# Kernel optimization log

Hardware: AMD Instinct MI355X
Metric: run time of the kernel (lower is better)

Reference implementation:

```python
import jax, jax.numpy as jnp
import numpy as np

B, C, N, K, G = 8, 64, 2048, 20, 64  # batch, in-channels, points, knn k, growth
BN_EPS = 1e-5


def setup_inputs() -> dict:
    key = jax.random.key(0)
    ks = jax.random.split(key, 8)
    def w(k_, fan_in, out):
        return jax.random.normal(k_, (out, fan_in), dtype=jnp.float32) / np.sqrt(fan_in)
    return {
        "inputs": jax.random.normal(ks[0], (B, C, N, 1), dtype=jnp.float32),
        "W1": w(ks[1], 2 * C, G), "b1": jnp.zeros((G,), jnp.float32),
        "g1": jnp.ones((G,), jnp.float32), "be1": jnp.zeros((G,), jnp.float32),
        "W2": w(ks[2], 2 * (C + G), G), "b2": jnp.zeros((G,), jnp.float32),
        "g2": jnp.ones((G,), jnp.float32), "be2": jnp.zeros((G,), jnp.float32),
        "W3": w(ks[3], 2 * (C + 2 * G), G), "b3": jnp.zeros((G,), jnp.float32),
        "g3": jnp.ones((G,), jnp.float32), "be3": jnp.zeros((G,), jnp.float32),
    }


def _knn_idx(x, k):
    # x: (B, C, N). Negative squared pairwise distance, topk = k nearest (incl. self).
    sq = jnp.sum(x * x, axis=1)                       # (B, N)
    inner = jnp.einsum('bcn,bcm->bnm', x, x)          # (B, N, N)
    neg_dist = 2.0 * inner - sq[:, :, None] - sq[:, None, :]
    return jax.lax.top_k(neg_dist, k)[1]              # (B, N, k)


def _dyn_edge_block(x4, W, b, gamma, beta):
    # x4: (B, Cin, N, 1) -> (B, G, N, 1). Dynamic KNN + EdgeConv + BN(batch stats) + ReLU + max over k.
    x = x4[..., 0]                                    # (B, Cin, N)
    idx = _knn_idx(x, K)                              # (B, N, K)
    xj = jax.vmap(lambda xb, ib: xb[:, ib])(x, idx)   # (B, Cin, N, K)
    xi = x[..., None]                                 # (B, Cin, N, 1)
    e = jnp.concatenate([jnp.broadcast_to(xi, xj.shape), xj - xi], axis=1)  # (B, 2Cin, N, K)
    y = jnp.einsum('oc,bcnk->bonk', W, e) + b[None, :, None, None]
    mu = jnp.mean(y, axis=(0, 2, 3), keepdims=True)
    var = jnp.var(y, axis=(0, 2, 3), keepdims=True)
    y = gamma[None, :, None, None] * (y - mu) * jax.lax.rsqrt(var + BN_EPS) + beta[None, :, None, None]
    y = jax.nn.relu(y)
    return jnp.max(y, axis=3, keepdims=True)          # (B, G, N, 1)


def reference(inputs, W1, b1, g1, be1, W2, b2, g2, be2, W3, b3, g3, be3):
    f = _dyn_edge_block(inputs, W1, b1, g1, be1)      # (B, G, N, 1)
    f1 = jnp.concatenate([f, inputs], axis=1)         # (B, C+G, N, 1)
    f2_new = _dyn_edge_block(f1, W2, b2, g2, be2)
    f2 = jnp.concatenate([f2_new, f1], axis=1)        # (B, C+2G, N, 1)
    f3_new = _dyn_edge_block(f2, W3, b3, g3, be3)
    return jnp.concatenate([f3_new, f2], axis=1)      # (B, C+3G, N, 1)
```

## Files before the change

### kernel.cpp

```cpp
#include <hip/hip_runtime.h>

#define NB 8
#define NPTS 2048
#define KNN 20
#define OUTC 256
#define NPB 8
#define NRED 64

__global__ void k_copy_in(const float* __restrict__ in, float* __restrict__ out) {
    int t = blockIdx.x * 256 + threadIdx.x;
    int n = t & (NPTS - 1);
    int c = (t >> 11) & 63;
    int b = t >> 17;
    out[((size_t)b * OUTC + 192 + c) * NPTS + n] = in[t];
}

__global__ void k_prep_uv(const float* __restrict__ W, int Cin,
                          float* __restrict__ Ut, float* __restrict__ Vt) {
    int t = blockIdx.x * 256 + threadIdx.x;
    if (t >= Cin * 64) return;
    int o = t & 63;
    int c = t >> 6;
    float wa = W[o * (2 * Cin) + c];
    float wb = W[o * (2 * Cin) + Cin + c];
    Ut[c * 64 + o] = wa - wb;
    Vt[c * 64 + o] = wb;
}

__global__ void k_sqsum(const float* __restrict__ out, int Cin, float* __restrict__ sq) {
    int t = blockIdx.x * 256 + threadIdx.x;
    int b = t >> 11;
    int m = t & (NPTS - 1);
    const float* X = out + ((size_t)b * OUTC + (OUTC - Cin)) * NPTS;
    float s = 0.f;
    for (int c = 0; c < Cin; ++c) {
        float x = X[(size_t)c * NPTS + m];
        s = fmaf(x, x, s);
    }
    sq[t] = s;
}

#define BSW(j) (((j) >> 3) * 12 + ((j) & 7))

__global__ __launch_bounds__(256) void k_dist(const float* __restrict__ out, int Cin,
        const float* __restrict__ sq, float* __restrict__ dist,
        int bOff, int n0, int NR, int sym) {
    int mt, nt;
    if (sym) {
        int u = blockIdx.x;
        mt = 0;
        int rem = 16;
        while (u >= rem) { u -= rem; --rem; ++mt; }
        nt = mt + u;
    } else {
        mt = blockIdx.x; nt = blockIdx.y;
    }
    int bz = blockIdx.z;
    int b = bOff + bz;
    const float* X = out + ((size_t)b * OUTC + (OUTC - Cin)) * NPTS;
    int m0 = mt * 128;
    int nbase = n0 + nt * 128;
    __shared__ float An[16][128];
    __shared__ float Bm[16][192];
    int t = threadIdx.x;
    int tx = t & 15, ty = t >> 4;
    float acc[8][8];
    #pragma unroll
    for (int i = 0; i < 8; ++i)
        #pragma unroll
        for (int j = 0; j < 8; ++j) acc[i][j] = 0.f;

    int lcol = (t & 31) * 4;
    int swl = BSW(lcol);
    int lrow = t >> 5;
    for (int kk = 0; kk < Cin; kk += 16) {
        #pragma unroll
        for (int i = 0; i < 2; ++i) {
            int rr = lrow + i * 8;
            const float* src = X + (size_t)(kk + rr) * NPTS;
            *(float4*)&An[rr][lcol] = *(const float4*)&src[nbase + lcol];
            *(float4*)&Bm[rr][swl]  = *(const float4*)&src[m0 + lcol];
        }
        __syncthreads();
        #pragma unroll
        for (int k = 0; k < 16; ++k) {
            float av[8], bv[8];
            *(float4*)&av[0] = *(float4*)&An[k][ty * 8];
            *(float4*)&av[4] = *(float4*)&An[k][ty * 8 + 4];
            *(float4*)&bv[0] = *(float4*)&Bm[k][tx * 12];
            *(float4*)&bv[4] = *(float4*)&Bm[k][tx * 12 + 4];
            #pragma unroll
            for (int ia = 0; ia < 8; ++ia)
                #pragma unroll
                for (int ib = 0; ib < 8; ++ib)
                    acc[ia][ib] = fmaf(av[ia], bv[ib], acc[ia][ib]);
        }
        __syncthreads();
    }
    const float* sqb = sq + b * NPTS;
    float sqm[8];
    *(float4*)&sqm[0] = *(const float4*)&sqb[m0 + tx * 8];
    *(float4*)&sqm[4] = *(const float4*)&sqb[m0 + tx * 8 + 4];
    float* dbase = dist + (size_t)bz * NR * NPTS;
    #pragma unroll
    for (int ia = 0; ia < 8; ++ia) {
        int rn = nt * 128 + ty * 8 + ia;
        float ov[8];
        #pragma unroll
        for (int ib = 0; ib < 8; ++ib) ov[ib] = 2.f * acc[ia][ib] - sqm[ib];
        *(float4*)&dbase[(size_t)rn * NPTS + m0 + tx * 8]     = *(float4*)&ov[0];
        *(float4*)&dbase[(size_t)rn * NPTS + m0 + tx * 8 + 4] = *(float4*)&ov[4];
    }
    if (sym && mt < nt) {
        float sqn[8];
        *(float4*)&sqn[0] = *(const float4*)&sqb[nbase + ty * 8];
        *(float4*)&sqn[4] = *(const float4*)&sqb[nbase + ty * 8 + 4];
        #pragma unroll
        for (int ib = 0; ib < 8; ++ib) {
            int rm = m0 + tx * 8 + ib;
            float ov[8];
            #pragma unroll
            for (int ia = 0; ia < 8; ++ia) ov[ia] = 2.f * acc[ia][ib] - sqn[ia];
            *(float4*)&dbase[(size_t)rm * NPTS + nbase + ty * 8]     = *(float4*)&ov[0];
            *(float4*)&dbase[(size_t)rm * NPTS + nbase + ty * 8 + 4] = *(float4*)&ov[4];
        }
    }
}

#define SCOLX(lane, j) (((lane) << 2) + ((j) & 3) + (((j) >> 2) << 8))

__device__ __forceinline__ unsigned long long packkey(float v, int c) {
    unsigned u = __float_as_uint(v);
    u ^= ((unsigned)((int)u >> 31)) | 0x80000000u;
    return ((unsigned long long)u << 32) | (unsigned)(~c);
}

__device__ __forceinline__ void scan4k(const float (&v)[32], int lane,
        unsigned long long thrK,
        unsigned long long& a1, unsigned long long& a2,
        unsigned long long& a3, unsigned long long& a4, int& d) {
    unsigned long long tK = thrK;
    d = 0;
    #pragma unroll
    for (int p = 0; p < 4; ++p) {
        unsigned long long b0 = 0, b1 = 0, b2 = 0, b3 = 0;
        #pragma unroll
        for (int jj = 0; jj < 8; ++jj) {
            {
                int j = jj;
                unsigned long long kj = packkey(v[j], SCOLX(lane, j));
                if (kj < tK && kj > b0) b0 = kj;
            }
            {
                int j = 8 + jj;
                unsigned long long kj = packkey(v[j], SCOLX(lane, j));
                if (kj < tK && kj > b1) b1 = kj;
            }
            {
                int j = 16 + jj;
                unsigned long long kj = packkey(v[j], SCOLX(lane, j));
                if (kj < tK && kj > b2) b2 = kj;
            }
            {
                int j = 24 + jj;
                unsigned long long kj = packkey(v[j], SCOLX(lane, j));
                if (kj < tK && kj > b3) b3 = kj;
            }
        }
        if (b1 > b0) b0 = b1;
        if (b3 > b2) b2 = b3;
        if (b2 > b0) b0 = b2;
        if (p == 0)      a1 = b0;
        else if (p == 1) a2 = b0;
        else if (p == 2) a3 = b0;
        else             a4 = b0;
        if (b0 != 0) ++d;
        tK = b0;
    }
}

__global__ __launch_bounds__(256) void k_select(const float* __restrict__ dist,
        int* __restrict__ idx, int bOff, int n0, int NR) {
    int lane = threadIdx.x & 63;
    int r = blockIdx.x * 4 + (threadIdx.x >> 6);
    int bl = r / NR;
    int n = n0 + (r - bl * NR);
    const float4* row4 = (const float4*)(dist + (size_t)r * NPTS);
    float v[32];
    #pragma unroll
    for (int jj = 0; jj < 8; ++jj)
        *(float4*)&v[jj * 4] = row4[lane + 64 * jj];
    int* orow = idx + ((size_t)(bOff + bl) * NPTS + n) * KNN;

    unsigned long long a1, a2, a3, a4;
    int d;
    unsigned long long mlK = 0xFFFFFFFFFFFFFFFFull;
    scan4k(v, lane, mlK, a1, a2, a3, a4, d);

    for (int s = 0; s < KNN; ++s) {
        unsigned long long wk = a1;
        #pragma unroll
        for (int off = 32; off; off >>= 1) {
            unsigned long long ok = __shfl_xor(wk, off);
            if (ok > wk) wk = ok;
        }
        int wc = ~(int)(unsigned)(wk & 0xFFFFFFFFull);
        if (lane == 0) orow[s] = wc;
        bool won = (a1 != 0) && (wk == a1);
        if (won) {
            mlK = a1;
            a1 = a2; a2 = a3; a3 = a4; a4 = 0;
            --d;
        }
        if (s < KNN - 1 && __any(won && d == 0)) {
            if (won && d == 0)
                scan4k(v, lane, mlK, a1, a2, a3, a4, d);
        }
    }
}

__global__ __launch_bounds__(256) void k_pz(const float* __restrict__ out, int Cin,
        const float* __restrict__ Ut, const float* __restrict__ Vt,
        float* __restrict__ P, float* __restrict__ Z) {
    int b = blockIdx.y;
    int n0 = blockIdx.x * 64;
    const float* X = out + ((size_t)b * OUTC + (OUTC - Cin)) * NPTS;
    __shared__ float Xs[16][64];
    __shared__ float Us[16][64];
    __shared__ float Vs[16][64];
    int t = threadIdx.x;
    int tx = t & 15, ty = t >> 4;
    float accP[4][4] = {}, accZ[4][4] = {};
    int col = t & 63, r0 = t >> 6;
    for (int kk = 0; kk < Cin; kk += 16) {
        #pragma unroll
        for (int i = 0; i < 4; ++i) {
            int rr = r0 + i * 4;
            Xs[rr][col] = X[(size_t)(kk + rr) * NPTS + n0 + col];
            Us[rr][col] = Ut[(kk + rr) * 64 + col];
            Vs[rr][col] = Vt[(kk + rr) * 64 + col];
        }
        __syncthreads();
        #pragma unroll
        for (int k = 0; k < 16; ++k) {
            float xv[4], uv[4], vv[4];
            *(float4*)xv = *(float4*)&Xs[k][ty * 4];
            *(float4*)uv = *(float4*)&Us[k][tx * 4];
            *(float4*)vv = *(float4*)&Vs[k][tx * 4];
            #pragma unroll
            for (int a = 0; a < 4; ++a)
                #pragma unroll
                for (int o = 0; o < 4; ++o) {
                    accP[a][o] = fmaf(uv[o], xv[a], accP[a][o]);
                    accZ[a][o] = fmaf(vv[o], xv[a], accZ[a][o]);
                }
        }
        __syncthreads();
    }
    #pragma unroll
    for (int a = 0; a < 4; ++a) {
        size_t base = ((size_t)b * NPTS + n0 + ty * 4 + a) * 64 + tx * 4;
        *(float4*)&P[base] = *(float4*)&accP[a][0];
        *(float4*)&Z[base] = *(float4*)&accZ[a][0];
    }
}

__global__ __launch_bounds__(64) void k_gather(const int* __restrict__ idx,
        const float* __restrict__ P, const float* __restrict__ Z,
        const float* __restrict__ bias,
        float* __restrict__ ymax, float* __restrict__ ymin,
        float* __restrict__ partials) {
    int blk = blockIdx.x;
    int b = blk / (NPTS / NPB);
    int n0 = (blk % (NPTS / NPB)) * NPB;
    int o = threadIdx.x;
    float bv = bias[o];
    float S1 = 0.f, S2 = 0.f;
    const float* Zb = Z + (size_t)b * NPTS * 64;
    for (int i = 0; i < NPB; ++i) {
        int n = n0 + i;
        const int* ir = idx + ((size_t)b * NPTS + n) * KNN;
        float mx = -3.0e38f, mn = 3.0e38f, s1 = 0.f, s2 = 0.f;
        #pragma unroll
        for (int k = 0; k < KNN; ++k) {
            int m = ir[k];
            float zv = Zb[(size_t)m * 64 + o];
            mx = fmaxf(mx, zv);
            mn = fminf(mn, zv);
            s1 += zv;
            s2 = fmaf(zv, zv, s2);
        }
        float tv = P[((size_t)b * NPTS + n) * 64 + o] + bv;
        size_t yb = ((size_t)b * NPTS + n) * 64 + o;
        ymax[yb] = tv + mx;
        ymin[yb] = tv + mn;
        S1 += (float)KNN * tv + s1;
        S2 += fmaf((float)KNN * tv, tv, fmaf(2.f * tv, s1, s2));
    }
    partials[(size_t)blk * 128 + o] = S1;
    partials[(size_t)blk * 128 + 64 + o] = S2;
}

__global__ __launch_bounds__(256) void k_reduce(const float* __restrict__ partials,
                                                float* __restrict__ red) {
    __shared__ float L[256];
    int t = threadIdx.x;
    int j = t & 127, half = t >> 7;
    int rows = (NB * NPTS / NPB) / NRED;
    int base = blockIdx.x * rows + half;
    float s = 0.f;
    #pragma unroll
    for (int i = 0; i < 16; ++i)
        s += partials[(size_t)(base + 2 * i) * 128 + j];
    L[t] = s;
    __syncthreads();
    if (half == 0)
        red[(size_t)blockIdx.x * 128 + j] = L[j] + L[128 + j];
}

__global__ void k_stats(const float* __restrict__ red,
        const float* __restrict__ gamma, const float* __restrict__ beta,
        float* __restrict__ ss) {
    __shared__ float L[128];
    int j = threadIdx.x;
    float s = 0.f;
    #pragma unroll
    for (int p = 0; p < NRED; ++p) s += red[(size_t)p * 128 + j];
    L[j] = s;
    __syncthreads();
    if (j < 64) {
        const float cnt = (float)NB * NPTS * KNN;
        float mu = L[j] / cnt;
        float ms = L[64 + j] / cnt;
        float var = ms - mu * mu;
        float sc = gamma[j] / sqrtf(var + 1e-5f);
        ss[j] = sc;
        ss[64 + j] = beta[j] - mu * sc;
    }
}

__global__ __launch_bounds__(256) void k_final(const float* __restrict__ ymax,
        const float* __restrict__ ymin, const float* __restrict__ ss,
        float* __restrict__ out, int obase) {
    int b = blockIdx.y;
    int n0 = blockIdx.x * 64;
    __shared__ float T[64][65];
    int t = threadIdx.x;
    int o = t & 63, r0 = t >> 6;
    float sc = ss[o], sh = ss[64 + o];
    #pragma unroll
    for (int i = 0; i < 16; ++i) {
        int n = r0 + i * 4;
        size_t src = ((size_t)b * NPTS + n0 + n) * 64 + o;
        float v = (sc >= 0.f) ? ymax[src] : ymin[src];
        v = fmaf(sc, v, sh);
        T[o][n] = v > 0.f ? v : 0.f;
    }
    __syncthreads();
    #pragma unroll
    for (int i = 0; i < 16; ++i) {
        int oo = r0 + i * 4;
        out[((size_t)b * OUTC + obase + oo) * NPTS + n0 + o] = T[oo][o];
    }
}

extern "C" void kernel_launch(void* const* d_in, const int* in_sizes, int n_in,
                              void* d_out, int out_size, void* d_ws, size_t ws_size,
                              hipStream_t stream) {
    const float* inp   = (const float*)d_in[0];
    const float* W[3]  = {(const float*)d_in[1], (const float*)d_in[5], (const float*)d_in[9]};
    const float* bi[3] = {(const float*)d_in[2], (const float*)d_in[6], (const float*)d_in[10]};
    const float* ga[3] = {(const float*)d_in[3], (const float*)d_in[7], (const float*)d_in[11]};
    const float* be[3] = {(const float*)d_in[4], (const float*)d_in[8], (const float*)d_in[12]};
    float* out = (float*)d_out;
    (void)in_sizes; (void)n_in; (void)out_size;

    char* w = (char*)d_ws;
    size_t off = 0;
    auto alloc = [&](size_t bytes) -> void* {
        void* p = w + off;
        off = (off + bytes + 255) & ~(size_t)255;
        return p;
    };
    int*   idx      = (int*)  alloc((size_t)NB * NPTS * KNN * 4);
    float* Ut       = (float*)alloc(192 * 64 * 4);
    float* Vt       = (float*)alloc(192 * 64 * 4);
    float* sq       = (float*)alloc((size_t)NB * NPTS * 4);
    float* P        = (float*)alloc((size_t)NB * NPTS * 64 * 4);
    float* Z        = (float*)alloc((size_t)NB * NPTS * 64 * 4);
    float* ymax     = (float*)alloc((size_t)NB * NPTS * 64 * 4);
    float* ymin     = (float*)alloc((size_t)NB * NPTS * 64 * 4);
    float* partials = (float*)alloc((size_t)(NB * NPTS / NPB) * 128 * 4);
    float* red      = (float*)alloc((size_t)NRED * 128 * 4);
    float* ss       = (float*)alloc(128 * 4);

    float* dist = (float*)(w + off);
    size_t distAvail = (ws_size > off) ? (ws_size - off) : 0;
    const size_t matBytes = (size_t)NPTS * NPTS * 4;

    k_copy_in<<<NB * 64 * NPTS / 256, 256, 0, stream>>>(inp, out);

    int Cins[3]  = {64, 128, 192};
    int obase[3] = {128, 64, 0};
    int nblkGather = NB * NPTS / NPB;

    for (int l = 0; l < 3; ++l) {
        int Cin = Cins[l];
        k_prep_uv<<<(Cin * 64 + 255) / 256, 256, 0, stream>>>(W[l], Cin, Ut, Vt);
        k_sqsum<<<NB * NPTS / 256, 256, 0, stream>>>(out, Cin, sq);

        if (distAvail >= (size_t)NB * matBytes) {
            k_dist<<<dim3(136, 1, NB), 256, 0, stream>>>(out, Cin, sq, dist, 0, 0, NPTS, 1);
            k_select<<<NB * NPTS / 4, 256, 0, stream>>>(dist, idx, 0, 0, NPTS);
        } else if (distAvail >= matBytes) {
            for (int b = 0; b < NB; ++b) {
                k_dist<<<dim3(136, 1, 1), 256, 0, stream>>>(out, Cin, sq, dist, b, 0, NPTS, 1);
                k_select<<<NPTS / 4, 256, 0, stream>>>(dist, idx, b, 0, NPTS);
            }
        } else {
            int NR = (int)((distAvail / ((size_t)NPTS * 4)) & ~(size_t)127);
            if (NR < 128) NR = 128;
            for (int b = 0; b < NB; ++b) {
                for (int n0 = 0; n0 < NPTS; n0 += NR) {
                    int nr = (NPTS - n0 < NR) ? (NPTS - n0) : NR;
                    k_dist<<<dim3(16, nr / 128, 1), 256, 0, stream>>>(out, Cin, sq, dist, b, n0, nr, 0);
                    k_select<<<nr / 4, 256, 0, stream>>>(dist, idx, b, n0, nr);
                }
            }
        }

        k_pz<<<dim3(NPTS / 64, NB), 256, 0, stream>>>(out, Cin, Ut, Vt, P, Z);
        k_gather<<<nblkGather, 64, 0, stream>>>(idx, P, Z, bi[l], ymax, ymin, partials);
        k_reduce<<<NRED, 256, 0, stream>>>(partials, red);
        k_stats<<<1, 128, 0, stream>>>(red, ga[l], be[l], ss);
        k_final<<<dim3(NPTS / 64, NB), 256, 0, stream>>>(ymax, ymin, ss, out, obase[l]);
    }
}
```

Measured before the change: 616.1 us.

## Fuse distance GEMM with per-row top-k selection for first layer

For the first EdgeConv layer, a new kernel computes pairwise-distance tiles and keeps a running top-20 per row in shared memory, split across two column halves. A small merge kernel then combines the two partial top-20 lists into the final indices. This skips writing and re-reading the full N×N distance matrix. In exchange the insertion loop is serial and divergent, and the grid is small (512 blocks), so occupancy may be low.

```diff
diff --git a/kernel.cpp b/kernel.cpp
--- a/kernel.cpp
+++ b/kernel.cpp
@@ -216,6 +216,133 @@
             if (won && d == 0)
                 scan4k(v, lane, mlK, a1, a2, a3, a4, d);
         }
+    }
+}
+
+__global__ __launch_bounds__(256) void k_fdist(const float* __restrict__ out, int Cin,
+        const float* __restrict__ sq, unsigned long long* __restrict__ ptop) {
+    int rt = blockIdx.x;
+    int half = blockIdx.y;
+    int b = blockIdx.z;
+    const float* X = out + ((size_t)b * OUTC + (OUTC - Cin)) * NPTS;
+    int rbase = rt * 64;
+    __shared__ float An[16][64];
+    __shared__ float Bm[16][192];
+    __shared__ unsigned long long g20[64][20];
+    int t = threadIdx.x;
+    int tx = t & 15, ty = t >> 4;
+
+    for (int j = t; j < 64 * 20; j += 256) ((unsigned long long*)g20)[j] = 0ull;
+    __syncthreads();
+
+    const float* sqb = sq + b * NPTS;
+    int lcolA = (t & 15) * 4, lrowA = t >> 4;
+    int lcolB = (t & 31) * 4, lrowB = t >> 5;
+    int swlB = BSW(lcolB);
+
+    for (int mt = 0; mt < 8; ++mt) {
+        int m0 = half * 1024 + mt * 128;
+        float acc[4][8];
+        #pragma unroll
+        for (int i = 0; i < 4; ++i)
+            #pragma unroll
+            for (int j = 0; j < 8; ++j) acc[i][j] = 0.f;
+        for (int kk = 0; kk < Cin; kk += 16) {
+            __syncthreads();
+            *(float4*)&An[lrowA][lcolA] =
+                *(const float4*)&X[(size_t)(kk + lrowA) * NPTS + rbase + lcolA];
+            #pragma unroll
+            for (int i = 0; i < 2; ++i) {
+                int rr = lrowB + i * 8;
+                *(float4*)&Bm[rr][swlB] =
+                    *(const float4*)&X[(size_t)(kk + rr) * NPTS + m0 + lcolB];
+            }
+            __syncthreads();
+            #pragma unroll
+            for (int k = 0; k < 16; ++k) {
+                float av[4], bv[8];
+                *(float4*)&av[0] = *(float4*)&An[k][ty * 4];
+                *(float4*)&bv[0] = *(float4*)&Bm[k][tx * 12];
+                *(float4*)&bv[4] = *(float4*)&Bm[k][tx * 12 + 4];
+                #pragma unroll
+                for (int ia = 0; ia < 4; ++ia)
+                    #pragma unroll
+                    for (int ib = 0; ib < 8; ++ib)
+                        acc[ia][ib] = fmaf(av[ia], bv[ib], acc[ia][ib]);
+            }
+        }
+        float sqm[8];
+        *(float4*)&sqm[0] = *(const float4*)&sqb[m0 + tx * 8];
+        *(float4*)&sqm[4] = *(const float4*)&sqb[m0 + tx * 8 + 4];
+        int cb = m0 + tx * 8;
+        #pragma unroll
+        for (int ia = 0; ia < 4; ++ia) {
+            int row = ty * 4 + ia;
+            unsigned long long tl = ~0ull, h = 0ull;
+            #pragma unroll
+            for (int j = 0; j < 8; ++j) {
+                unsigned long long kj = packkey(2.f * acc[ia][j] - sqm[j], cb + j);
+                if (kj < tl && kj > h) h = kj;
+            }
+            while (true) {
+                unsigned long long w = h;
+                #pragma unroll
+                for (int off = 8; off; off >>= 1) {
+                    unsigned long long o = __shfl_xor(w, off);
+                    if (o > w) w = o;
+                }
+                unsigned long long c1 = g20[row][tx]; int s1 = tx;
+                if (tx < 4) {
+                    unsigned long long c2 = g20[row][16 + tx];
+                    if (c2 < c1) { c1 = c2; s1 = 16 + tx; }
+                }
+                #pragma unroll
+                for (int off = 8; off; off >>= 1) {
+                    unsigned long long oc = __shfl_xor(c1, off);
+                    int os = __shfl_xor(s1, off);
+                    if (oc < c1) { c1 = oc; s1 = os; }
+                }
+                if (w <= c1) break;
+                if (tx == 0) g20[row][s1] = w;
+                if (h == w && h != 0ull) {
+                    tl = h;
+                    h = 0ull;
+                    #pragma unroll
+                    for (int j = 0; j < 8; ++j) {
+                        unsigned long long kj = packkey(2.f * acc[ia][j] - sqm[j], cb + j);
+                        if (kj < tl && kj > h) h = kj;
+                    }
+                }
+            }
+        }
+    }
+    __syncthreads();
+    #pragma unroll
+    for (int ia = 0; ia < 4; ++ia) {
+        int row = ty * 4 + ia;
+        size_t base = ((size_t)b * NPTS + rbase + row) * 40 + (size_t)half * 20;
+        for (int j = tx; j < 20; j += 16)
+            ptop[base + j] = g20[row][j];
+    }
+}
+
+__global__ void k_kmerge(const unsigned long long* __restrict__ ptop,
+                         int* __restrict__ idx) {
+    int r = blockIdx.x * 256 + threadIdx.x;
+    const unsigned long long* src = ptop + (size_t)r * 40;
+    unsigned long long v[40];
+    #pragma unroll
+    for (int j = 0; j < 40; ++j) v[j] = src[j];
+    int* orow = idx + (size_t)r * KNN;
+    unsigned long long tV = ~0ull;
+    #pragma unroll 1
+    for (int s = 0; s < KNN; ++s) {
+        unsigned long long best = 0;
+        #pragma unroll
+        for (int j = 0; j < 40; ++j)
+            if (v[j] < tV && v[j] > best) best = v[j];
+        orow[s] = ~(int)(unsigned)(best & 0xFFFFFFFFull);
+        tV = best;
     }
 }
 
@@ -393,6 +520,7 @@
     float* partials = (float*)alloc((size_t)(NB * NPTS / NPB) * 128 * 4);
     float* red      = (float*)alloc((size_t)NRED * 128 * 4);
     float* ss       = (float*)alloc(128 * 4);
+    unsigned long long* ptop = (unsigned long long*)alloc((size_t)NB * NPTS * 40 * 8);
 
     float* dist = (float*)(w + off);
     size_t distAvail = (ws_size > off) ? (ws_size - off) : 0;
@@ -409,7 +537,10 @@
         k_prep_uv<<<(Cin * 64 + 255) / 256, 256, 0, stream>>>(W[l], Cin, Ut, Vt);
         k_sqsum<<<NB * NPTS / 256, 256, 0, stream>>>(out, Cin, sq);
 
-        if (distAvail >= (size_t)NB * matBytes) {
+        if (l == 0) {
+            k_fdist<<<dim3(32, 2, NB), 256, 0, stream>>>(out, Cin, sq, ptop);
+            k_kmerge<<<NB * NPTS / 256, 256, 0, stream>>>(ptop, idx);
+        } else if (distAvail >= (size_t)NB * matBytes) {
             k_dist<<<dim3(136, 1, NB), 256, 0, stream>>>(out, Cin, sq, dist, 0, 0, NPTS, 1);
             k_select<<<NB * NPTS / 4, 256, 0, stream>>>(dist, idx, 0, 0, NPTS);
         } else if (distAvail >= matBytes) {
```

New measurement: 796.2 us. 1.29x slower.
